# Kernel tuning notes

Hardware: AMD Instinct MI355X
Metric: run time of the kernel (lower is better)

Reference implementation:

```python
import jax, jax.numpy as jnp
import numpy as np

B = 2048   # jets (graphs)
P = 50     # particles per jet
N = B * P  # nodes
E = B * P * P  # within-jet all-pairs radius-graph edges (incl. self-loops)
H = 5      # edge-MLP width ([5,5,5,5] channel list)
EPS = 1e-5
NEG_SLOPE = 0.01


def _batchnorm(h, gamma, beta):
    # training-mode batch norm over the edge dimension (biased variance, as torch)
    mu = jnp.mean(h, axis=0)
    var = jnp.mean(h * h, axis=0) - mu * mu
    return gamma * (h - mu) * jax.lax.rsqrt(var + EPS) + beta


def setup_inputs() -> dict:
    key = jax.random.key(0)
    ks = jax.random.split(key, 16)
    # angles: per-jet center offset + tight spread so all within-jet pairs are inside dR=0.4
    centers = jax.random.normal(ks[0], (B, 1, 2), dtype=jnp.float32) + jnp.array([2.0, 0.5], dtype=jnp.float32)
    angles = (centers + 0.1 * jax.random.normal(ks[1], (B, P, 2), dtype=jnp.float32)).reshape(N, 2)
    pt = jax.random.uniform(ks[2], (N,), dtype=jnp.float32, minval=0.1, maxval=1.0)
    features = jnp.linalg.norm(angles, axis=-1, keepdims=True)  # rho = |view_as_complex(angles)|, [N,1]
    # radius graph: with the tight spread every within-jet pair is within dR -> fixed E
    ii = np.arange(P)
    pi, pj = np.meshgrid(ii, ii, indexing='ij')
    base = (np.arange(B, dtype=np.int64) * P)[:, None]
    src = (base + pj.ravel()[None, :]).ravel()  # x_j (source)
    dst = (base + pi.ravel()[None, :]).ravel()  # x_i (target) = aggregation index
    edge_index = jnp.asarray(np.stack([src, dst]), dtype=jnp.int32)  # [2, E]
    def lin(k, o, i):
        return (jax.random.normal(k, (o, i), dtype=jnp.float32) / np.sqrt(i)).astype(jnp.float32)
    W1 = lin(ks[3], H, 5); b1 = jnp.zeros((H,), jnp.float32)
    W2 = lin(ks[4], H, H); b2 = jnp.zeros((H,), jnp.float32)
    W3 = lin(ks[5], H, H); b3 = jnp.zeros((H,), jnp.float32)
    g1 = jnp.ones((H,), jnp.float32); bt1 = jnp.zeros((H,), jnp.float32)
    g2 = jnp.ones((H,), jnp.float32); bt2 = jnp.zeros((H,), jnp.float32)
    return {"pt": pt, "features": features, "angles": angles,
            "W1": W1, "b1": b1, "g1": g1, "bt1": bt1,
            "W2": W2, "b2": b2, "g2": g2, "bt2": bt2,
            "W3": W3, "b3": b3, "edge_index": edge_index}


def reference(pt, features, angles, W1, b1, g1, bt1, W2, b2, g2, bt2, W3, b3, edge_index):
    src = edge_index[0]  # j (source)
    dst = edge_index[1]  # i (target, aggregation index)
    x = jnp.concatenate([pt[:, None], features, angles], axis=1)  # [N, 4]
    xi = x[dst]  # [E, 4]
    xj = x[src]
    # complex ratio angles_i / angles_j in real arithmetic
    ar, ai = xi[:, 2], xi[:, 3]
    br, bi = xj[:, 2], xj[:, 3]
    den = br * br + bi * bi
    dr = (ar * br + ai * bi) / den
    di = (ai * br - ar * bi) / den
    fi = xi[:, 1:2]
    fj = xj[:, 1:2]
    mlp_in = jnp.concatenate([fi, fj, fj - fi, dr[:, None], di[:, None]], axis=1)  # [E, 5]
    h = jax.nn.leaky_relu(_batchnorm(mlp_in @ W1.T + b1, g1, bt1), NEG_SLOPE)
    h = jax.nn.leaky_relu(_batchnorm(h @ W2.T + b2, g2, bt2), NEG_SLOPE)
    h = h @ W3.T + b3  # [E, 5]
    msg = jnp.concatenate([xi[:, :1], h, xi[:, 2:4]], axis=1)  # [E, 8]
    pt_e = msg[:, 0]
    denom = jax.ops.segment_sum(pt_e, dst, num_segments=N)  # [N]
    wj = pt_e / denom[dst]
    agg = jax.ops.segment_sum(wj[:, None] * msg, dst, num_segments=N)  # [N, 8]
    # exp(2*pi*i*theta) * z with theta = agg[:, -3], z = complex(agg[:, -2:])
    theta = agg[:, 5]
    zr, zi = agg[:, 6], agg[:, 7]
    c = jnp.cos(2.0 * jnp.pi * theta)
    s = jnp.sin(2.0 * jnp.pi * theta)
    out = jnp.concatenate([agg[:, :5], (c * zr - s * zi)[:, None], (c * zi + s * zr)[:, None]], axis=1)  # [N, 7]
    return out
```

## Files before the change

### kernel.cpp

```cpp
#include <hip/hip_runtime.h>

#define PP 50
#define TPB 256
#define NBATCH 2048
#define GB 2
#define NBLK2 (NBATCH / GB)
#define NBLK1 512
#define NCOPY 16

static constexpr float EPSF = 1e-5f;
static constexpr double INV_ETOT = 1.0 / 5120000.0;

static __device__ __forceinline__ float lrelu(float x) {
    return fmaxf(x, 0.0f) + 0.01f * fminf(x, 0.0f);
}
static __device__ __forceinline__ float rfl(float x) {
    return __int_as_float(__builtin_amdgcn_readfirstlane(__float_as_int(x)));
}


__global__ __launch_bounds__(TPB) void stats1_kernel(
    const float* __restrict__ feat, const float* __restrict__ ang,
    const float* __restrict__ W1, const float* __restrict__ b1,
    double* __restrict__ acc)
{
    __shared__ double bacc[4][10];
    const int t = threadIdx.x;
    const int lane = t & 63;
    const int wv = t >> 6;

    float v0[5], v1[5], v2[5], v3[5], bb1[5];
#pragma unroll
    for (int o = 0; o < 5; ++o) {
        v0[o] = rfl(W1[o*5+0] - W1[o*5+2]);
        v1[o] = rfl(W1[o*5+1] + W1[o*5+2]);
        v2[o] = rfl(W1[o*5+3]);
        v3[o] = rfl(W1[o*5+4]);
        bb1[o] = rfl(b1[o]);
    }

    float f = 0.f, zr = 0.f, zi = 0.f, inv = 0.f;
    if (lane < PP) {
        const int idx = (blockIdx.x * 4 + wv) * PP + lane;
        f = feat[idx];
        float2 a2 = ((const float2*)ang)[idx];
        zr = a2.x; zi = a2.y;
        inv = 1.0f / (zr*zr + zi*zi);
    }
    const float wr = zr * inv, wi = -zi * inv;

    float p[16] = { f, f*f, zr, zi, wr, wi, f*zr, f*zi, f*wr, f*wi,
                    zr*zr, zi*zi, zr*zi, wr*wr, wi*wi, wr*wi };
#pragma unroll
    for (int k = 0; k < 16; ++k) {
        float v = p[k];
#pragma unroll
        for (int off = 32; off > 0; off >>= 1) v += __shfl_down(v, off, 64);
        p[k] = v;
    }
    if (lane == 0) {
        const double P0 = p[0], P1 = p[1], P2 = p[2], P3 = p[3], P4 = p[4];
        const double P5 = p[5], P6 = p[6], P7 = p[7], P8 = p[8], P9 = p[9];
        const double P10 = p[10], P11 = p[11], P12 = p[12];
        const double P13 = p[13], P14 = p[14], P15 = p[15];
        const double Sfi = 50.0 * P0;
        const double Sdr = P2*P4 - P3*P5;
        const double Sdi = P3*P4 + P2*P5;
        const double m00 = 50.0 * P1, m11 = m00, m01 = P0*P0;
        const double m02 = P6*P4 - P7*P5;
        const double m03 = P7*P4 + P6*P5;
        const double m12 = P2*P8 - P3*P9;
        const double m13 = P3*P8 + P2*P9;
        const double m22 = P10*P13 - 2.0*P12*P15 + P11*P14;
        const double m33 = P11*P13 + 2.0*P12*P15 + P10*P14;
        const double m23 = P12*P13 + P10*P15 - P11*P15 - P12*P14;
#pragma unroll
        for (int o = 0; o < 5; ++o) {
            const double a0=v0[o], a1=v1[o], a2=v2[o], a3=v3[o], bo=bb1[o];
            const double sy = a0*Sfi + a1*Sfi + a2*Sdr + a3*Sdi + 2500.0*bo;
            const double q  = a0*a0*m00 + a1*a1*m11 + a2*a2*m22 + a3*a3*m33
                           + 2.0*(a0*a1*m01 + a0*a2*m02 + a0*a3*m03
                                + a1*a2*m12 + a1*a3*m13 + a2*a3*m23);
            bacc[wv][o]   = sy;
            bacc[wv][5+o] = q + 2.0*bo*sy - 2500.0*bo*bo;
        }
    }
    __syncthreads();
    if (t < 10) {
        double s = bacc[0][t] + bacc[1][t] + bacc[2][t] + bacc[3][t];
        atomicAdd(&acc[t * NCOPY + (blockIdx.x & (NCOPY-1))], s);
    }
}

__global__ __launch_bounds__(TPB) void pass2_kernel(
    const float* __restrict__ feat, const float* __restrict__ ang,
    const float* __restrict__ W1, const float* __restrict__ b1,
    const float* __restrict__ g1, const float* __restrict__ bt1,
    const float* __restrict__ W2, const float* __restrict__ b2,
    double* __restrict__ acc)
{
    __shared__ float4 nd[GB][PP];
    __shared__ double tmp[10];
    __shared__ float red[4][10];
    const int t = threadIdx.x;

    if (t < PP) {
        const int idx = blockIdx.x * GB * PP + t;
        float f = feat[idx];
        float2 a2 = ((const float2*)ang)[idx];
        nd[0][t] = make_float4(f, a2.x, a2.y, 1.0f / (a2.x*a2.x + a2.y*a2.y));
    } else if (t >= 64 && t < 64 + PP) {
        const int idx = blockIdx.x * GB * PP + PP + (t - 64);
        float f = feat[idx];
        float2 a2 = ((const float2*)ang)[idx];
        nd[1][t-64] = make_float4(f, a2.x, a2.y, 1.0f / (a2.x*a2.x + a2.y*a2.y));
    } else if (t >= 128 && t < 138) {
        const int k = t - 128;
        double s = 0.0;
#pragma unroll
        for (int c = 0; c < NCOPY; ++c) s += acc[k * NCOPY + c];
        tmp[k] = s;
    }

    float v0[5], v1[5], v2[5], v3[5], bb1[5], w2[25], bb2[5];
#pragma unroll
    for (int o = 0; o < 5; ++o) {
        v0[o] = rfl(W1[o*5+0] - W1[o*5+2]);
        v1[o] = rfl(W1[o*5+1] + W1[o*5+2]);
        v2[o] = rfl(W1[o*5+3]);
        v3[o] = rfl(W1[o*5+4]);
        bb1[o] = rfl(b1[o]); bb2[o] = rfl(b2[o]);
    }
#pragma unroll
    for (int i = 0; i < 25; ++i) w2[i] = rfl(W2[i]);

    __syncthreads();

    float sc1[5], sh1[5];
#pragma unroll
    for (int o = 0; o < 5; ++o) {
        double mu  = tmp[o]   * INV_ETOT;
        double var = tmp[5+o] * INV_ETOT - mu * mu;
        float sc = rfl(g1[o]) * rsqrtf((float)var + EPSF);
        sc1[o] = rfl(sc);
        sh1[o] = rfl(rfl(bt1[o]) - (float)mu * sc);
    }

    float a[10];
#pragma unroll
    for (int k = 0; k < 10; ++k) a[k] = 0.f;

    if (t < 250) {
        const int pi = t / 5;
        const int s5 = t - pi*5;
#pragma unroll
        for (int g = 0; g < GB; ++g) {
            const float4 ni = nd[g][pi];
            const float fi = ni.x, ari = ni.y, aii = ni.z;
#pragma unroll
            for (int q = 0; q < 10; ++q) {
                const float4 nj = nd[g][s5*10 + q];
                const float dr = fmaf(ari, nj.y,  aii*nj.z) * nj.w;
                const float di = fmaf(aii, nj.y, -ari*nj.z) * nj.w;
                float h1[5];
#pragma unroll
                for (int o = 0; o < 5; ++o) {
                    float y = fmaf(v0[o], fi, fmaf(v1[o], nj.x,
                              fmaf(v2[o], dr, fmaf(v3[o], di, bb1[o]))));
                    h1[o] = lrelu(fmaf(y, sc1[o], sh1[o]));
                }
#pragma unroll
                for (int o = 0; o < 5; ++o) {
                    float y = bb2[o];
                    y = fmaf(w2[o*5+0], h1[0], y);
                    y = fmaf(w2[o*5+1], h1[1], y);
                    y = fmaf(w2[o*5+2], h1[2], y);
                    y = fmaf(w2[o*5+3], h1[3], y);
                    y = fmaf(w2[o*5+4], h1[4], y);
                    a[o]   += y;
                    a[5+o]  = fmaf(y, y, a[5+o]);
                }
            }
        }
    }

#pragma unroll
    for (int k = 0; k < 10; ++k) {
        float v = a[k];
#pragma unroll
        for (int off = 32; off > 0; off >>= 1) v += __shfl_down(v, off, 64);
        a[k] = v;
    }
    const int lane = t & 63, wv = t >> 6;
    if (lane == 0) {
#pragma unroll
        for (int k = 0; k < 10; ++k) red[wv][k] = a[k];
    }
    __syncthreads();
    if (t < 10) {
        atomicAdd(&acc[(10 + t) * NCOPY + (blockIdx.x & (NCOPY-1))],
                  (double)(red[0][t] + red[1][t] + red[2][t] + red[3][t]));
    }
}

__global__ __launch_bounds__(TPB) void pass3_kernel(
    const float* __restrict__ pt,
    const float* __restrict__ feat, const float* __restrict__ ang,
    const float* __restrict__ W1, const float* __restrict__ b1,
    const float* __restrict__ g1, const float* __restrict__ bt1,
    const float* __restrict__ W2, const float* __restrict__ b2,
    const float* __restrict__ g2, const float* __restrict__ bt2,
    const float* __restrict__ W3, const float* __restrict__ b3,
    const double* __restrict__ acc, float* __restrict__ out)
{
    __shared__ float4 nd[GB][PP];
    __shared__ float spt[GB][PP];
    __shared__ double tmp[20];
    __shared__ float part[250][5];
    const int t = threadIdx.x;

    if (t < PP) {
        const int idx = blockIdx.x * GB * PP + t;
        float f = feat[idx];
        float2 a2 = ((const float2*)ang)[idx];
        nd[0][t] = make_float4(f, a2.x, a2.y, 1.0f / (a2.x*a2.x + a2.y*a2.y));
        spt[0][t] = pt[idx];
    } else if (t >= 64 && t < 64 + PP) {
        const int idx = blockIdx.x * GB * PP + PP + (t - 64);
        float f = feat[idx];
        float2 a2 = ((const float2*)ang)[idx];
        nd[1][t-64] = make_float4(f, a2.x, a2.y, 1.0f / (a2.x*a2.x + a2.y*a2.y));
        spt[1][t-64] = pt[idx];
    } else if (t >= 128 && t < 148) {
        const int k = t - 128;
        double s = 0.0;
#pragma unroll
        for (int c = 0; c < NCOPY; ++c) s += acc[k * NCOPY + c];
        tmp[k] = s;
    }

    float v0[5], v1[5], v2[5], v3[5], bb1[5], w2[25], bb2[5], w3[25], bb3[5];
#pragma unroll
    for (int o = 0; o < 5; ++o) {
        v0[o] = rfl(W1[o*5+0] - W1[o*5+2]);
        v1[o] = rfl(W1[o*5+1] + W1[o*5+2]);
        v2[o] = rfl(W1[o*5+3]);
        v3[o] = rfl(W1[o*5+4]);
        bb1[o] = rfl(b1[o]); bb2[o] = rfl(b2[o]); bb3[o] = rfl(b3[o]);
    }
#pragma unroll
    for (int i = 0; i < 25; ++i) { w2[i] = rfl(W2[i]); w3[i] = rfl(W3[i]); }

    __syncthreads();

    float sc1[5], sh1[5], sc2[5], sh2[5];
#pragma unroll
    for (int o = 0; o < 5; ++o) {
        double mu1  = tmp[o]    * INV_ETOT;
        double var1 = tmp[5+o]  * INV_ETOT - mu1 * mu1;
        float s1 = rfl(g1[o]) * rsqrtf((float)var1 + EPSF);
        sc1[o] = rfl(s1);
        sh1[o] = rfl(rfl(bt1[o]) - (float)mu1 * s1);
        double mu2  = tmp[10+o] * INV_ETOT;
        double var2 = tmp[15+o] * INV_ETOT - mu2 * mu2;
        float s2 = rfl(g2[o]) * rsqrtf((float)var2 + EPSF);
        sc2[o] = rfl(s2);
        sh2[o] = rfl(rfl(bt2[o]) - (float)mu2 * s2);
    }

    const int pi = t / 5;
    const int s5 = t - pi*5;

#pragma unroll
    for (int g = 0; g < GB; ++g) {
        float a[5] = {0.f, 0.f, 0.f, 0.f, 0.f};
        if (t < 250) {
            const float4 ni = nd[g][pi];
            const float fi = ni.x, ari = ni.y, aii = ni.z;
#pragma unroll
            for (int q = 0; q < 10; ++q) {
                const float4 nj = nd[g][s5*10 + q];
                const float dr = fmaf(ari, nj.y,  aii*nj.z) * nj.w;
                const float di = fmaf(aii, nj.y, -ari*nj.z) * nj.w;
                float h1[5], h2[5];
#pragma unroll
                for (int o = 0; o < 5; ++o) {
                    float y = fmaf(v0[o], fi, fmaf(v1[o], nj.x,
                              fmaf(v2[o], dr, fmaf(v3[o], di, bb1[o]))));
                    h1[o] = lrelu(fmaf(y, sc1[o], sh1[o]));
                }
#pragma unroll
                for (int o = 0; o < 5; ++o) {
                    float y = bb2[o];
                    y = fmaf(w2[o*5+0], h1[0], y);
                    y = fmaf(w2[o*5+1], h1[1], y);
                    y = fmaf(w2[o*5+2], h1[2], y);
                    y = fmaf(w2[o*5+3], h1[3], y);
                    y = fmaf(w2[o*5+4], h1[4], y);
                    h2[o] = lrelu(fmaf(y, sc2[o], sh2[o]));
                }
#pragma unroll
                for (int o = 0; o < 5; ++o) {
                    float y = bb3[o];
                    y = fmaf(w3[o*5+0], h2[0], y);
                    y = fmaf(w3[o*5+1], h2[1], y);
                    y = fmaf(w3[o*5+2], h2[2], y);
                    y = fmaf(w3[o*5+3], h2[3], y);
                    y = fmaf(w3[o*5+4], h2[4], y);
                    a[o] += y;
                }
            }
#pragma unroll
            for (int c = 0; c < 5; ++c) part[t][c] = a[c];
        }
        __syncthreads();

        if (t < PP) {
            float m[5];
#pragma unroll
            for (int c = 0; c < 5; ++c) {
                m[c] = (part[5*t][c] + part[5*t+1][c] + part[5*t+2][c] +
                        part[5*t+3][c] + part[5*t+4][c]) * 0.02f;
            }
            const int d = (blockIdx.x * GB + g) * PP + t;
            const float4 ni = nd[g][t];
            float ss, cc;
            sincosf(6.2831853071795865f * m[4], &ss, &cc);
            float* o = out + (size_t)d * 7;
            o[0] = spt[g][t];
            o[1] = m[0];
            o[2] = m[1];
            o[3] = m[2];
            o[4] = m[3];
            o[5] = cc * ni.y - ss * ni.z;
            o[6] = cc * ni.z + ss * ni.y;
        }
        __syncthreads();
    }
}

extern "C" void kernel_launch(void* const* d_in, const int* in_sizes, int n_in,
                              void* d_out, int out_size, void* d_ws, size_t ws_size,
                              hipStream_t stream)
{
    const float* pt   = (const float*)d_in[0];
    const float* feat = (const float*)d_in[1];
    const float* ang  = (const float*)d_in[2];
    const float* W1   = (const float*)d_in[3];
    const float* b1   = (const float*)d_in[4];
    const float* g1   = (const float*)d_in[5];
    const float* bt1  = (const float*)d_in[6];
    const float* W2   = (const float*)d_in[7];
    const float* b2   = (const float*)d_in[8];
    const float* g2   = (const float*)d_in[9];
    const float* bt2  = (const float*)d_in[10];
    const float* W3   = (const float*)d_in[11];
    const float* b3   = (const float*)d_in[12];
    float* out  = (float*)d_out;
    double* acc = (double*)d_ws;

    hipMemsetAsync(d_ws, 0, 20 * NCOPY * sizeof(double), stream);
    stats1_kernel<<<NBLK1, TPB, 0, stream>>>(feat, ang, W1, b1, acc);
    pass2_kernel<<<NBLK2, TPB, 0, stream>>>(feat, ang, W1, b1, g1, bt1, W2, b2, acc);
    pass3_kernel<<<NBLK2, TPB, 0, stream>>>(pt, feat, ang, W1, b1, g1, bt1, W2, b2,
                                            g2, bt2, W3, b3, acc, out);
}
```

Before: 146.3 us.

## Map one wavefront per jet with a lane per target node

The two MLP passes now give each jet its own 64-lane wavefront. Each lane owns one target particle and loops over all 50 sources. This replaces the old layout of five threads per target with a shared-memory partial reduction and block barriers. The block-wide stat reads are replaced by per-lane loads and wave shuffles over 64 accumulator copies, and atomics are issued per wave. This removes block syncs and the shared partial-sum step, but leaves 14 of 64 lanes idle and halves the total wave count. It also relies on implicit intra-wave ordering for the shared node table.

Result: slower. 151.9 us (+3.8%).

```diff
diff --git a/kernel.cpp b/kernel.cpp
--- a/kernel.cpp
+++ b/kernel.cpp
@@ -3,10 +3,9 @@
 #define PP 50
 #define TPB 256
 #define NBATCH 2048
-#define GB 2
-#define NBLK2 (NBATCH / GB)
-#define NBLK1 512
-#define NCOPY 16
+#define WPB 4
+#define NBLK (NBATCH / WPB)
+#define NCOPY 64
 
 static constexpr float EPSF = 1e-5f;
 static constexpr double INV_ETOT = 1.0 / 5120000.0;
@@ -41,7 +40,7 @@
 
     float f = 0.f, zr = 0.f, zi = 0.f, inv = 0.f;
     if (lane < PP) {
-        const int idx = (blockIdx.x * 4 + wv) * PP + lane;
+        const int idx = (blockIdx.x * WPB + wv) * PP + lane;
         f = feat[idx];
         float2 a2 = ((const float2*)ang)[idx];
         zr = a2.x; zi = a2.y;
@@ -99,27 +98,18 @@
     const float* __restrict__ W2, const float* __restrict__ b2,
     double* __restrict__ acc)
 {
-    __shared__ float4 nd[GB][PP];
-    __shared__ double tmp[10];
-    __shared__ float red[4][10];
+    __shared__ float4 snd[WPB][PP];
     const int t = threadIdx.x;
-
-    if (t < PP) {
-        const int idx = blockIdx.x * GB * PP + t;
-        float f = feat[idx];
+    const int lane = t & 63;
+    const int wv = t >> 6;
+    const int batch = blockIdx.x * WPB + wv;
+
+    float f = 0.f, zr = 0.f, zi = 0.f;
+    if (lane < PP) {
+        const int idx = batch * PP + lane;
+        f = feat[idx];
         float2 a2 = ((const float2*)ang)[idx];
-        nd[0][t] = make_float4(f, a2.x, a2.y, 1.0f / (a2.x*a2.x + a2.y*a2.y));
-    } else if (t >= 64 && t < 64 + PP) {
-        const int idx = blockIdx.x * GB * PP + PP + (t - 64);
-        float f = feat[idx];
-        float2 a2 = ((const float2*)ang)[idx];
-        nd[1][t-64] = make_float4(f, a2.x, a2.y, 1.0f / (a2.x*a2.x + a2.y*a2.y));
-    } else if (t >= 128 && t < 138) {
-        const int k = t - 128;
-        double s = 0.0;
-#pragma unroll
-        for (int c = 0; c < NCOPY; ++c) s += acc[k * NCOPY + c];
-        tmp[k] = s;
+        zr = a2.x; zi = a2.y;
     }
 
     float v0[5], v1[5], v2[5], v3[5], bb1[5], w2[25], bb2[5];
@@ -134,72 +124,71 @@
 #pragma unroll
     for (int i = 0; i < 25; ++i) w2[i] = rfl(W2[i]);
 
-    __syncthreads();
-
+    double tp[10];
+#pragma unroll
+    for (int s = 0; s < 10; ++s) tp[s] = acc[s * NCOPY + lane];
+#pragma unroll
+    for (int s = 0; s < 10; ++s) {
+#pragma unroll
+        for (int off = 32; off > 0; off >>= 1) tp[s] += __shfl_xor(tp[s], off, 64);
+    }
     float sc1[5], sh1[5];
 #pragma unroll
     for (int o = 0; o < 5; ++o) {
-        double mu  = tmp[o]   * INV_ETOT;
-        double var = tmp[5+o] * INV_ETOT - mu * mu;
+        double mu  = tp[o]   * INV_ETOT;
+        double var = tp[5+o] * INV_ETOT - mu * mu;
         float sc = rfl(g1[o]) * rsqrtf((float)var + EPSF);
         sc1[o] = rfl(sc);
         sh1[o] = rfl(rfl(bt1[o]) - (float)mu * sc);
     }
 
+    if (lane < PP) {
+        snd[wv][lane] = make_float4(f, zr, zi, 1.0f / (zr*zr + zi*zi));
+    }
+
+    const float fi = f, ari = zr, aii = zi;
     float a[10];
 #pragma unroll
     for (int k = 0; k < 10; ++k) a[k] = 0.f;
 
-    if (t < 250) {
-        const int pi = t / 5;
-        const int s5 = t - pi*5;
-#pragma unroll
-        for (int g = 0; g < GB; ++g) {
-            const float4 ni = nd[g][pi];
-            const float fi = ni.x, ari = ni.y, aii = ni.z;
-#pragma unroll
-            for (int q = 0; q < 10; ++q) {
-                const float4 nj = nd[g][s5*10 + q];
-                const float dr = fmaf(ari, nj.y,  aii*nj.z) * nj.w;
-                const float di = fmaf(aii, nj.y, -ari*nj.z) * nj.w;
-                float h1[5];
-#pragma unroll
-                for (int o = 0; o < 5; ++o) {
-                    float y = fmaf(v0[o], fi, fmaf(v1[o], nj.x,
-                              fmaf(v2[o], dr, fmaf(v3[o], di, bb1[o]))));
-                    h1[o] = lrelu(fmaf(y, sc1[o], sh1[o]));
-                }
-#pragma unroll
-                for (int o = 0; o < 5; ++o) {
-                    float y = bb2[o];
-                    y = fmaf(w2[o*5+0], h1[0], y);
-                    y = fmaf(w2[o*5+1], h1[1], y);
-                    y = fmaf(w2[o*5+2], h1[2], y);
-                    y = fmaf(w2[o*5+3], h1[3], y);
-                    y = fmaf(w2[o*5+4], h1[4], y);
-                    a[o]   += y;
-                    a[5+o]  = fmaf(y, y, a[5+o]);
-                }
-            }
-        }
-    }
-
+#pragma unroll 10
+    for (int pj = 0; pj < PP; ++pj) {
+        const float4 nj = snd[wv][pj];
+        const float dr = fmaf(ari, nj.y,  aii*nj.z) * nj.w;
+        const float di = fmaf(aii, nj.y, -ari*nj.z) * nj.w;
+        float h1[5];
+#pragma unroll
+        for (int o = 0; o < 5; ++o) {
+            float y = fmaf(v0[o], fi, fmaf(v1[o], nj.x,
+                      fmaf(v2[o], dr, fmaf(v3[o], di, bb1[o]))));
+            h1[o] = lrelu(fmaf(y, sc1[o], sh1[o]));
+        }
+#pragma unroll
+        for (int o = 0; o < 5; ++o) {
+            float y = bb2[o];
+            y = fmaf(w2[o*5+0], h1[0], y);
+            y = fmaf(w2[o*5+1], h1[1], y);
+            y = fmaf(w2[o*5+2], h1[2], y);
+            y = fmaf(w2[o*5+3], h1[3], y);
+            y = fmaf(w2[o*5+4], h1[4], y);
+            a[o]   += y;
+            a[5+o]  = fmaf(y, y, a[5+o]);
+        }
+    }
+    if (lane >= PP) {
+#pragma unroll
+        for (int k = 0; k < 10; ++k) a[k] = 0.f;
+    }
 #pragma unroll
     for (int k = 0; k < 10; ++k) {
-        float v = a[k];
-#pragma unroll
-        for (int off = 32; off > 0; off >>= 1) v += __shfl_down(v, off, 64);
-        a[k] = v;
-    }
-    const int lane = t & 63, wv = t >> 6;
+#pragma unroll
+        for (int off = 32; off > 0; off >>= 1) a[k] += __shfl_xor(a[k], off, 64);
+    }
     if (lane == 0) {
-#pragma unroll
-        for (int k = 0; k < 10; ++k) red[wv][k] = a[k];
-    }
-    __syncthreads();
-    if (t < 10) {
-        atomicAdd(&acc[(10 + t) * NCOPY + (blockIdx.x & (NCOPY-1))],
-                  (double)(red[0][t] + red[1][t] + red[2][t] + red[3][t]));
+        const int copy = batch & (NCOPY - 1);
+#pragma unroll
+        for (int s = 0; s < 10; ++s)
+            atomicAdd(&acc[(10 + s) * NCOPY + copy], (double)a[s]);
     }
 }
 
@@ -213,30 +202,19 @@
     const float* __restrict__ W3, const float* __restrict__ b3,
     const double* __restrict__ acc, float* __restrict__ out)
 {
-    __shared__ float4 nd[GB][PP];
-    __shared__ float spt[GB][PP];
-    __shared__ double tmp[20];
-    __shared__ float part[250][5];
+    __shared__ float4 snd[WPB][PP];
     const int t = threadIdx.x;
-
-    if (t < PP) {
-        const int idx = blockIdx.x * GB * PP + t;
-        float f = feat[idx];
+    const int lane = t & 63;
+    const int wv = t >> 6;
+    const int batch = blockIdx.x * WPB + wv;
+
+    float f = 0.f, zr = 0.f, zi = 0.f, mypt = 0.f;
+    if (lane < PP) {
+        const int idx = batch * PP + lane;
+        f = feat[idx];
         float2 a2 = ((const float2*)ang)[idx];
-        nd[0][t] = make_float4(f, a2.x, a2.y, 1.0f / (a2.x*a2.x + a2.y*a2.y));
-        spt[0][t] = pt[idx];
-    } else if (t >= 64 && t < 64 + PP) {
-        const int idx = blockIdx.x * GB * PP + PP + (t - 64);
-        float f = feat[idx];
-        float2 a2 = ((const float2*)ang)[idx];
-        nd[1][t-64] = make_float4(f, a2.x, a2.y, 1.0f / (a2.x*a2.x + a2.y*a2.y));
-        spt[1][t-64] = pt[idx];
-    } else if (t >= 128 && t < 148) {
-        const int k = t - 128;
-        double s = 0.0;
-#pragma unroll
-        for (int c = 0; c < NCOPY; ++c) s += acc[k * NCOPY + c];
-        tmp[k] = s;
+        zr = a2.x; zi = a2.y;
+        mypt = pt[idx];
     }
 
     float v0[5], v1[5], v2[5], v3[5], bb1[5], w2[25], bb2[5], w3[25], bb3[5];
@@ -251,91 +229,84 @@
 #pragma unroll
     for (int i = 0; i < 25; ++i) { w2[i] = rfl(W2[i]); w3[i] = rfl(W3[i]); }
 
-    __syncthreads();
-
+    double tp[20];
+#pragma unroll
+    for (int s = 0; s < 20; ++s) tp[s] = acc[s * NCOPY + lane];
+#pragma unroll
+    for (int s = 0; s < 20; ++s) {
+#pragma unroll
+        for (int off = 32; off > 0; off >>= 1) tp[s] += __shfl_xor(tp[s], off, 64);
+    }
     float sc1[5], sh1[5], sc2[5], sh2[5];
 #pragma unroll
     for (int o = 0; o < 5; ++o) {
-        double mu1  = tmp[o]    * INV_ETOT;
-        double var1 = tmp[5+o]  * INV_ETOT - mu1 * mu1;
+        double mu1  = tp[o]    * INV_ETOT;
+        double var1 = tp[5+o]  * INV_ETOT - mu1 * mu1;
         float s1 = rfl(g1[o]) * rsqrtf((float)var1 + EPSF);
         sc1[o] = rfl(s1);
         sh1[o] = rfl(rfl(bt1[o]) - (float)mu1 * s1);
-        double mu2  = tmp[10+o] * INV_ETOT;
-        double var2 = tmp[15+o] * INV_ETOT - mu2 * mu2;
+        double mu2  = tp[10+o] * INV_ETOT;
+        double var2 = tp[15+o] * INV_ETOT - mu2 * mu2;
         float s2 = rfl(g2[o]) * rsqrtf((float)var2 + EPSF);
         sc2[o] = rfl(s2);
         sh2[o] = rfl(rfl(bt2[o]) - (float)mu2 * s2);
     }
 
-    const int pi = t / 5;
-    const int s5 = t - pi*5;
-
-#pragma unroll
-    for (int g = 0; g < GB; ++g) {
-        float a[5] = {0.f, 0.f, 0.f, 0.f, 0.f};
-        if (t < 250) {
-            const float4 ni = nd[g][pi];
-            const float fi = ni.x, ari = ni.y, aii = ni.z;
-#pragma unroll
-            for (int q = 0; q < 10; ++q) {
-                const float4 nj = nd[g][s5*10 + q];
-                const float dr = fmaf(ari, nj.y,  aii*nj.z) * nj.w;
-                const float di = fmaf(aii, nj.y, -ari*nj.z) * nj.w;
-                float h1[5], h2[5];
-#pragma unroll
-                for (int o = 0; o < 5; ++o) {
-                    float y = fmaf(v0[o], fi, fmaf(v1[o], nj.x,
-                              fmaf(v2[o], dr, fmaf(v3[o], di, bb1[o]))));
-                    h1[o] = lrelu(fmaf(y, sc1[o], sh1[o]));
-                }
-#pragma unroll
-                for (int o = 0; o < 5; ++o) {
-                    float y = bb2[o];
-                    y = fmaf(w2[o*5+0], h1[0], y);
-                    y = fmaf(w2[o*5+1], h1[1], y);
-                    y = fmaf(w2[o*5+2], h1[2], y);
-                    y = fmaf(w2[o*5+3], h1[3], y);
-                    y = fmaf(w2[o*5+4], h1[4], y);
-                    h2[o] = lrelu(fmaf(y, sc2[o], sh2[o]));
-                }
-#pragma unroll
-                for (int o = 0; o < 5; ++o) {
-                    float y = bb3[o];
-                    y = fmaf(w3[o*5+0], h2[0], y);
-                    y = fmaf(w3[o*5+1], h2[1], y);
-                    y = fmaf(w3[o*5+2], h2[2], y);
-                    y = fmaf(w3[o*5+3], h2[3], y);
-                    y = fmaf(w3[o*5+4], h2[4], y);
-                    a[o] += y;
-                }
-            }
-#pragma unroll
-            for (int c = 0; c < 5; ++c) part[t][c] = a[c];
-        }
-        __syncthreads();
-
-        if (t < PP) {
-            float m[5];
-#pragma unroll
-            for (int c = 0; c < 5; ++c) {
-                m[c] = (part[5*t][c] + part[5*t+1][c] + part[5*t+2][c] +
-                        part[5*t+3][c] + part[5*t+4][c]) * 0.02f;
-            }
-            const int d = (blockIdx.x * GB + g) * PP + t;
-            const float4 ni = nd[g][t];
-            float ss, cc;
-            sincosf(6.2831853071795865f * m[4], &ss, &cc);
-            float* o = out + (size_t)d * 7;
-            o[0] = spt[g][t];
-            o[1] = m[0];
-            o[2] = m[1];
-            o[3] = m[2];
-            o[4] = m[3];
-            o[5] = cc * ni.y - ss * ni.z;
-            o[6] = cc * ni.z + ss * ni.y;
-        }
-        __syncthreads();
+    if (lane < PP) {
+        snd[wv][lane] = make_float4(f, zr, zi, 1.0f / (zr*zr + zi*zi));
+    }
+
+    const float fi = f, ari = zr, aii = zi;
+    float m[5] = {0.f, 0.f, 0.f, 0.f, 0.f};
+
+#pragma unroll 10
+    for (int pj = 0; pj < PP; ++pj) {
+        const float4 nj = snd[wv][pj];
+        const float dr = fmaf(ari, nj.y,  aii*nj.z) * nj.w;
+        const float di = fmaf(aii, nj.y, -ari*nj.z) * nj.w;
+        float h1[5], h2[5];
+#pragma unroll
+        for (int o = 0; o < 5; ++o) {
+            float y = fmaf(v0[o], fi, fmaf(v1[o], nj.x,
+                      fmaf(v2[o], dr, fmaf(v3[o], di, bb1[o]))));
+            h1[o] = lrelu(fmaf(y, sc1[o], sh1[o]));
+        }
+#pragma unroll
+        for (int o = 0; o < 5; ++o) {
+            float y = bb2[o];
+            y = fmaf(w2[o*5+0], h1[0], y);
+            y = fmaf(w2[o*5+1], h1[1], y);
+            y = fmaf(w2[o*5+2], h1[2], y);
+            y = fmaf(w2[o*5+3], h1[3], y);
+            y = fmaf(w2[o*5+4], h1[4], y);
+            h2[o] = lrelu(fmaf(y, sc2[o], sh2[o]));
+        }
+#pragma unroll
+        for (int o = 0; o < 5; ++o) {
+            float y = bb3[o];
+            y = fmaf(w3[o*5+0], h2[0], y);
+            y = fmaf(w3[o*5+1], h2[1], y);
+            y = fmaf(w3[o*5+2], h2[2], y);
+            y = fmaf(w3[o*5+3], h2[3], y);
+            y = fmaf(w3[o*5+4], h2[4], y);
+            m[o] += y;
+        }
+    }
+
+    if (lane < PP) {
+#pragma unroll
+        for (int c = 0; c < 5; ++c) m[c] *= 0.02f;
+        float ss, cc;
+        sincosf(6.2831853071795865f * m[4], &ss, &cc);
+        const int d = batch * PP + lane;
+        float* o = out + (size_t)d * 7;
+        o[0] = mypt;
+        o[1] = m[0];
+        o[2] = m[1];
+        o[3] = m[2];
+        o[4] = m[3];
+        o[5] = cc * zr - ss * zi;
+        o[6] = cc * zi + ss * zr;
     }
 }
 
@@ -360,8 +331,8 @@
     double* acc = (double*)d_ws;
 
     hipMemsetAsync(d_ws, 0, 20 * NCOPY * sizeof(double), stream);
-    stats1_kernel<<<NBLK1, TPB, 0, stream>>>(feat, ang, W1, b1, acc);
-    pass2_kernel<<<NBLK2, TPB, 0, stream>>>(feat, ang, W1, b1, g1, bt1, W2, b2, acc);
-    pass3_kernel<<<NBLK2, TPB, 0, stream>>>(pt, feat, ang, W1, b1, g1, bt1, W2, b2,
-                                            g2, bt2, W3, b3, acc, out);
-}
+    stats1_kernel<<<NBLK, TPB, 0, stream>>>(feat, ang, W1, b1, acc);
+    pass2_kernel<<<NBLK, TPB, 0, stream>>>(feat, ang, W1, b1, g1, bt1, W2, b2, acc);
+    pass3_kernel<<<NBLK, TPB, 0, stream>>>(pt, feat, ang, W1, b1, g1, bt1, W2, b2,
+                                           g2, bt2, W3, b3, acc, out);
+}
```
